# Kernel optimization log

Measured on AMD Instinct MI355X. Metric: run time of the kernel, lower is better.

The kernel has to match this reference:

```python
import jax, jax.numpy as jnp
import numpy as np

NEG = -1e30  # log(0) surrogate, safe for fp32
BLANK = 0
MARGIN = 16.0
EPS = 1e-6  # torch pairwise_distance eps


def ctc_loss(log_probs, labels, input_lengths, label_lengths):
    """Per-sample CTC negative log-likelihood (== nn.CTCLoss(blank=0, reduction='none')).
    log_probs: (T, N, C) log-probabilities; labels: (N, S) int; lengths: (N,).
    """
    T, N, C = log_probs.shape
    S = labels.shape[1]
    L = 2 * S + 1  # extended label length (blanks interleaved)

    # extended labels: blank at even positions, labels at odd positions
    ext = jnp.zeros((N, L), dtype=labels.dtype).at[:, 1::2].set(labels)  # (N, L)
    # skip transition s-2 -> s allowed iff ext[s] != blank and ext[s] != ext[s-2]
    skip = jnp.concatenate(
        [jnp.zeros((N, 2), dtype=bool),
         (ext[:, 2:] != ext[:, :-2]) & (ext[:, 2:] != BLANK)], axis=1)  # (N, L)

    def emit(lp_t):  # lp_t: (N, C) -> (N, L) log-prob of each extended symbol
        return jnp.take_along_axis(lp_t, ext, axis=1)

    # t = 0 init: only positions 0 (blank) and 1 (first label) reachable
    e0 = emit(log_probs[0])
    alpha0 = jnp.full((N, L), NEG).at[:, 0].set(e0[:, 0]).at[:, 1].set(e0[:, 1])

    def step(alpha, xs):
        t, lp_t = xs
        prev1 = jnp.concatenate([jnp.full((N, 1), NEG), alpha[:, :-1]], axis=1)
        prev2 = jnp.concatenate([jnp.full((N, 2), NEG), alpha[:, :-2]], axis=1)
        a = jnp.logaddexp(jnp.logaddexp(alpha, prev1),
                          jnp.where(skip, prev2, NEG)) + emit(lp_t)
        # freeze alpha once t >= input_length (per sample)
        a = jnp.where((t < input_lengths)[:, None], a, alpha)
        return a, None

    ts = jnp.arange(1, T)
    alpha_T, _ = jax.lax.scan(step, alpha0, (ts, log_probs[1:]))

    # final: logaddexp(alpha[2L], alpha[2L-1]) at last valid frame
    idx_hi = (2 * label_lengths)[:, None]
    a_hi = jnp.take_along_axis(alpha_T, idx_hi, axis=1)[:, 0]
    a_lo = jnp.take_along_axis(alpha_T, idx_hi - 1, axis=1)[:, 0]
    return -jnp.logaddexp(a_hi, a_lo)  # (N,)


def setup_inputs() -> dict:
    key = jax.random.key(0)
    k1, k2, k3, k4, k5 = jax.random.split(key, 5)
    T, N, C, S = 1024, 128, 256, 100
    predicts = jax.nn.log_softmax(
        jax.random.normal(k1, (T, N, C), dtype=jnp.float32), axis=-1)
    labels = jax.random.randint(k2, (N, S), 1, C, dtype=jnp.int32)
    ref_labels = jax.random.randint(k3, (N, S), 1, C, dtype=jnp.int32)
    preds_lengths = jnp.full((N,), T, dtype=jnp.int32)
    label_lengths = jax.random.randint(k4, (N,), 50, S + 1, dtype=jnp.int32)
    ref_lengths = jax.random.randint(k5, (N,), 50, S + 1, dtype=jnp.int32)
    return {"predicts": predicts, "labels": labels, "ref_labels": ref_labels,
            "preds_lengths": preds_lengths, "label_lengths": label_lengths,
            "ref_lengths": ref_lengths}


def reference(predicts, labels, ref_labels, preds_lengths, label_lengths, ref_lengths):
    ctc = ctc_loss(predicts, labels, preds_lengths, label_lengths)      # (N,)
    ref = ctc_loss(predicts, ref_labels, preds_lengths, ref_lengths)    # (N,)
    # TripletMarginLoss(margin=16, p=2), anchor = 0, 1-d embeddings:
    # d(a,x) = |0 - x + eps| ; reduction='mean'; .sum() on scalar is identity.
    d_ap = jnp.abs(EPS - ctc)
    d_an = jnp.abs(EPS - ref)
    margin_loss = jnp.mean(jnp.maximum(d_ap - d_an + MARGIN, 0.0))
    return ctc.sum() + margin_loss
```

## Files before the change

kernel.cpp:

```cpp
#include <hip/hip_runtime.h>
#include <math.h>

#define LOG2E 1.4426950408889634f
#define LN2F  0.6931471805599453f
#define NEGB  (-1e30f)

__device__ __forceinline__ float fexp2(float x){ float r; asm("v_exp_f32 %0, %1":"=v"(r):"v"(x)); return r; }
__device__ __forceinline__ float flog2(float x){ float r; asm("v_log_f32 %0, %1":"=v"(r):"v"(x)); return r; }

template<int CTRL>
__device__ __forceinline__ float dppf(float x){
    return __int_as_float(__builtin_amdgcn_update_dpp(0, __float_as_int(x), CTRL, 0xf, 0xf, false));
}

__global__ __launch_bounds__(64) void ctc_scan_kernel(
    const float* __restrict__ lp,
    const int* __restrict__ labels,
    const int* __restrict__ rlabels,
    const int* __restrict__ ilen,
    const int* __restrict__ llen,
    const int* __restrict__ rlen,
    float* __restrict__ loss,
    int T, int N, int C, int S)
{
    const int n    = blockIdx.x >> 1;
    const int sq   = blockIdx.x & 1;
    const int lane = threadIdx.x;

    const int* lab = sq ? rlabels : labels;
    const int  ll  = sq ? rlen[n] : llen[n];
    int Teff = ilen[n]; if (Teff > T) Teff = T;
    const int Tm1 = T - 1;

    int e1 = 0, e3 = 0;
    bool k1 = false, k3 = false;
    {
        int j0 = 2*lane, j1 = 2*lane + 1;
        if (j0 < S){ e1 = lab[n*S + j0]; if (j0 > 0) k1 = (e1 != lab[n*S + j0 - 1]); }
        if (j1 < S){ e3 = lab[n*S + j1]; k3 = (e3 != e1); }
    }
    const float m0 = (2*lane     <= ll) ? 1.f : 0.f;
    const float m2 = (2*lane + 1 <= ll) ? 1.f : 0.f;
    const float b1 = (2*lane     <  ll) ? 0.f : NEGB;
    const float b3 = (2*lane + 1 <  ll) ? 0.f : NEGB;
    const bool bnd = ((lane & 15) == 0) && (lane != 0);

    const size_t NC = (size_t)N * C;
    const float* base = lp + (size_t)n * C;

    float a0, a1, a2 = 0.f, a3 = 0.f;
    {
        float pb0 = fexp2(base[0]  * LOG2E);
        float p10 = fexp2(base[e1] * LOG2E);
        a0 = (lane == 0) ? pb0 : 0.f;
        a1 = (lane == 0) ? p10 : 0.f;
    }
    int E = 0;

    float Rb[4][3], Rx[4][3], Ry[4][3];
#pragma unroll
    for (int q = 0; q < 4; ++q)
#pragma unroll
        for (int u = 0; u < 3; ++u){
            int tt = 1 + q*3 + u; tt = tt < T ? tt : Tm1;
            const float* rp = base + (size_t)tt * NC;
            Rb[q][u] = rp[0] * LOG2E;
            Rx[q][u] = fmaf(rp[e1], LOG2E, b1);
            Ry[q][u] = fmaf(rp[e3], LOG2E, b3);
        }

    auto stepf = [&](float PB, float PX, float PY){
        float pb = fexp2(PB);
        float p1 = fexp2(PX);
        float p3 = fexp2(PY);
        float sh = dppf<0x111>(a3);
        float bc = dppf<0x142>(a3);
        float pa3 = bnd ? bc : sh;
        float v0 = (a0 + pa3) * (pb * m0);
        float v1 = (a1 + a0 + (k1 ? pa3 : 0.f)) * p1;
        float v2 = (a2 + a1) * (pb * m2);
        float v3 = (a3 + a2 + (k3 ? a1 : 0.f)) * p3;
        a0 = v0; a1 = v1; a2 = v2; a3 = v3;
    };

    auto rescale = [&](){
        float m = fmaxf(fmaxf(a0, a1), fmaxf(a2, a3));
        m = fmaxf(m, dppf<0x111>(m));
        m = fmaxf(m, dppf<0x112>(m));
        m = fmaxf(m, dppf<0x114>(m));
        m = fmaxf(m, dppf<0x118>(m));
        m = fmaxf(m, dppf<0x142>(m));
        m = fmaxf(m, dppf<0x143>(m));
        float wmax = __int_as_float(__builtin_amdgcn_readlane(__float_as_int(m), 63));
        int ex = ((__float_as_int(wmax) >> 23) & 255) - 127;
        a0 = ldexpf(a0, -ex); a1 = ldexpf(a1, -ex);
        a2 = ldexpf(a2, -ex); a3 = ldexpf(a3, -ex);
        E += ex;
    };

    int t = 1;
    for (; t + 12 <= Teff; t += 12){
#pragma unroll
        for (int q = 0; q < 4; ++q){
#pragma unroll
            for (int u = 0; u < 3; ++u) stepf(Rb[q][u], Rx[q][u], Ry[q][u]);
#pragma unroll
            for (int u = 0; u < 3; ++u){
                int tt = t + 12 + q*3 + u; tt = tt < T ? tt : Tm1;
                const float* rp = base + (size_t)tt * NC;
                Rb[q][u] = rp[0] * LOG2E;
                Rx[q][u] = fmaf(rp[e1], LOG2E, b1);
                Ry[q][u] = fmaf(rp[e3], LOG2E, b3);
            }
            if (q & 1) rescale();
        }
    }
#pragma unroll
    for (int i = 0; i < 12; ++i){
        if (t + i < Teff) stepf(Rb[i/3][i%3], Rx[i/3][i%3], Ry[i/3][i%3]);
    }

    __shared__ __align__(16) float aout[256];
    reinterpret_cast<float4*>(aout)[lane] = make_float4(a0, a1, a2, a3);
    __syncthreads();
    if (lane == 0){
        float hi = aout[2*ll], lo = aout[2*ll - 1];
        loss[sq * N + n] = -(flog2(hi + lo) + (float)E) * LN2F;
    }
}

__global__ __launch_bounds__(256) void ctc_finalize_kernel(
    const float* __restrict__ ws, float* __restrict__ out, int N)
{
    __shared__ float sc[256], sh[256];
    const int i = threadIdx.x;
    float c = 0.f, h = 0.f;
    for (int nn = i; nn < N; nn += 256) {
        float cv = ws[nn];
        float rv = ws[N + nn];
        c += cv;
        float dap = fabsf(1e-6f - cv);
        float dan = fabsf(1e-6f - rv);
        h += fmaxf(dap - dan + 16.0f, 0.f);
    }
    sc[i] = c; sh[i] = h;
    __syncthreads();
    for (int off = 128; off > 0; off >>= 1) {
        if (i < off) { sc[i] += sc[i + off]; sh[i] += sh[i + off]; }
        __syncthreads();
    }
    if (i == 0) out[0] = sc[0] + sh[0] / (float)N;
}

extern "C" void kernel_launch(void* const* d_in, const int* in_sizes, int n_in,
                              void* d_out, int out_size, void* d_ws, size_t ws_size,
                              hipStream_t stream) {
    const float* lp      = (const float*)d_in[0];
    const int* labels    = (const int*)d_in[1];
    const int* rlabels   = (const int*)d_in[2];
    const int* plen      = (const int*)d_in[3];
    const int* llen      = (const int*)d_in[4];
    const int* rlen      = (const int*)d_in[5];

    const int N = in_sizes[3];
    const int S = in_sizes[1] / N;
    const int C = 256;
    const int T = in_sizes[0] / (N * C);

    float* ws = (float*)d_ws;

    ctc_scan_kernel<<<2 * N, 64, 0, stream>>>(lp, labels, rlabels, plen, llen, rlen,
                                              ws, T, N, C, S);
    ctc_finalize_kernel<<<1, 256, 0, stream>>>(ws, (float*)d_out, N);
}
```

Baseline: 115.6 us.

## Hand-schedule deeper prefetch pipeline with inline asm loads and explicit vmcnt waits

Raises the prefetch depth of log-prob rows from 12 to 18 timesteps and issues the loads through inline-asm global_load_dword with an SGPR base. Partial s_waitcnt vmcnt(45) waits and sched barriers let the recurrence consume the oldest group while later loads stay in flight. The LOG2E scaling and the blank mask fmas move from load time into the step. The aim is to hide global memory latency on the serial scan, at the cost of more registers and fragile hand-tuned wait counts.

```diff
diff --git a/kernel.cpp b/kernel.cpp
--- a/kernel.cpp
+++ b/kernel.cpp
@@ -12,6 +12,16 @@
 __device__ __forceinline__ float dppf(float x){
     return __int_as_float(__builtin_amdgcn_update_dpp(0, __float_as_int(x), CTRL, 0xf, 0xf, false));
 }
+
+__device__ __forceinline__ float gload(const float* sbase, int voff){
+    float r;
+    asm volatile("global_load_dword %0, %1, %2"
+                 : "=v"(r) : "v"(voff), "s"(sbase));
+    return r;
+}
+
+#define WAITV(N) asm volatile("s_waitcnt vmcnt(" #N ")" ::: "memory")
+#define SB0() __builtin_amdgcn_sched_barrier(0)
 
 __global__ __launch_bounds__(64) void ctc_scan_kernel(
     const float* __restrict__ lp,
@@ -47,6 +57,7 @@
 
     const size_t NC = (size_t)N * C;
     const float* base = lp + (size_t)n * C;
+    const int vx = 4*e1, vy = 4*e3, vz = 0;
 
     float a0, a1, a2 = 0.f, a3 = 0.f;
     {
@@ -57,22 +68,25 @@
     }
     int E = 0;
 
-    float Rb[4][3], Rx[4][3], Ry[4][3];
+    asm volatile("s_waitcnt vmcnt(0)" ::: "memory");
+    SB0();
+
+    float Rb[6][3], Rx[6][3], Ry[6][3];
 #pragma unroll
-    for (int q = 0; q < 4; ++q)
+    for (int g = 0; g < 6; ++g)
 #pragma unroll
         for (int u = 0; u < 3; ++u){
-            int tt = 1 + q*3 + u; tt = tt < T ? tt : Tm1;
-            const float* rp = base + (size_t)tt * NC;
-            Rb[q][u] = rp[0] * LOG2E;
-            Rx[q][u] = fmaf(rp[e1], LOG2E, b1);
-            Ry[q][u] = fmaf(rp[e3], LOG2E, b3);
+            int row = 1 + g*3 + u; if (row > Tm1) row = Tm1;
+            const float* rp = base + (size_t)row * NC;
+            Rb[g][u] = gload(rp, vz);
+            Rx[g][u] = gload(rp, vx);
+            Ry[g][u] = gload(rp, vy);
         }
 
     auto stepf = [&](float PB, float PX, float PY){
-        float pb = fexp2(PB);
-        float p1 = fexp2(PX);
-        float p3 = fexp2(PY);
+        float pb = fexp2(PB * LOG2E);
+        float p1 = fexp2(fmaf(PX, LOG2E, b1));
+        float p3 = fexp2(fmaf(PY, LOG2E, b3));
         float sh = dppf<0x111>(a3);
         float bc = dppf<0x142>(a3);
         float pa3 = bnd ? bc : sh;
@@ -99,25 +113,34 @@
     };
 
     int t = 1;
-    for (; t + 12 <= Teff; t += 12){
+    for (; t + 18 <= Teff; t += 18){
 #pragma unroll
-        for (int q = 0; q < 4; ++q){
-#pragma unroll
-            for (int u = 0; u < 3; ++u) stepf(Rb[q][u], Rx[q][u], Ry[q][u]);
+        for (int g = 0; g < 6; ++g){
+            WAITV(45);
+            SB0();
+            stepf(Rb[g][0], Rx[g][0], Ry[g][0]);
+            stepf(Rb[g][1], Rx[g][1], Ry[g][1]);
+            stepf(Rb[g][2], Rx[g][2], Ry[g][2]);
+            if (g & 1) rescale();
 #pragma unroll
             for (int u = 0; u < 3; ++u){
-                int tt = t + 12 + q*3 + u; tt = tt < T ? tt : Tm1;
-                const float* rp = base + (size_t)tt * NC;
-                Rb[q][u] = rp[0] * LOG2E;
-                Rx[q][u] = fmaf(rp[e1], LOG2E, b1);
-                Ry[q][u] = fmaf(rp[e3], LOG2E, b3);
+                int row = t + 18 + g*3 + u; if (row > Tm1) row = Tm1;
+                const float* rp = base + (size_t)row * NC;
+                Rb[g][u] = gload(rp, vz);
+                Rx[g][u] = gload(rp, vx);
+                Ry[g][u] = gload(rp, vy);
             }
-            if (q & 1) rescale();
         }
     }
+
+    WAITV(0);
+    SB0();
 #pragma unroll
-    for (int i = 0; i < 12; ++i){
-        if (t + i < Teff) stepf(Rb[i/3][i%3], Rx[i/3][i%3], Ry[i/3][i%3]);
+    for (int g = 0; g < 6; ++g){
+#pragma unroll
+        for (int u = 0; u < 3; ++u)
+            if (t + g*3 + u < Teff) stepf(Rb[g][u], Rx[g][u], Ry[g][u]);
+        if (t + g*3 < Teff) rescale();
     }
 
     __shared__ __align__(16) float aout[256];
```

Measured after the change: 102.2 us. -11.6%, faster.

## Stage per-timestep log-prob rows into an LDS ring via async global_load_lds

Applied to the files above, without the earlier changes.

Replaces the per-lane register prefetch of scattered gathered log-probs with coalesced async global-to-LDS copies of whole 256-class rows into a 32-deep ring buffer, 24 rows ahead. Each step then reads its blank and label emissions from LDS, with hand-placed waitcnt and sched barriers to overlap loads with the recurrence. The goal is to replace the latency-bound scattered global gathers on the serial critical path. In exchange it relies on fragile manual vmcnt/lgkmcnt counting, loads full rows instead of only the needed entries, and now rescales every 6 steps instead of 2.

```diff
diff --git a/kernel.cpp b/kernel.cpp
--- a/kernel.cpp
+++ b/kernel.cpp
@@ -12,6 +12,16 @@
 __device__ __forceinline__ float dppf(float x){
     return __int_as_float(__builtin_amdgcn_update_dpp(0, __float_as_int(x), CTRL, 0xf, 0xf, false));
 }
+
+__device__ __forceinline__ float ldsread(unsigned addr){
+    float r;
+    asm volatile("ds_read_b32 %0, %1" : "=v"(r) : "v"(addr));
+    return r;
+}
+
+#define WAITV(N) asm volatile("s_waitcnt vmcnt(" #N ")" ::: "memory")
+#define WAITL(N) asm volatile("s_waitcnt lgkmcnt(" #N ")" ::: "memory")
+#define SB0() __builtin_amdgcn_sched_barrier(0)
 
 __global__ __launch_bounds__(64) void ctc_scan_kernel(
     const float* __restrict__ lp,
@@ -32,6 +42,9 @@
     int Teff = ilen[n]; if (Teff > T) Teff = T;
     const int Tm1 = T - 1;
 
+    __shared__ __align__(16) float ring[32][256];
+    __shared__ __align__(16) float aout[256];
+
     int e1 = 0, e3 = 0;
     bool k1 = false, k3 = false;
     {
@@ -47,6 +60,12 @@
 
     const size_t NC = (size_t)N * C;
     const float* base = lp + (size_t)n * C;
+    const float* gsrc = base + lane * 4;
+
+    const unsigned RB = (unsigned)(size_t)(__attribute__((address_space(3))) char*)&ring[0][0];
+    const unsigned ab = RB;
+    const unsigned ax = RB + 4u * (unsigned)e1;
+    const unsigned ay = RB + 4u * (unsigned)e3;
 
     float a0, a1, a2 = 0.f, a3 = 0.f;
     {
@@ -57,22 +76,29 @@
     }
     int E = 0;
 
-    float Rb[4][3], Rx[4][3], Ry[4][3];
-#pragma unroll
-    for (int q = 0; q < 4; ++q)
-#pragma unroll
-        for (int u = 0; u < 3; ++u){
-            int tt = 1 + q*3 + u; tt = tt < T ? tt : Tm1;
-            const float* rp = base + (size_t)tt * NC;
-            Rb[q][u] = rp[0] * LOG2E;
-            Rx[q][u] = fmaf(rp[e1], LOG2E, b1);
-            Ry[q][u] = fmaf(rp[e3], LOG2E, b3);
-        }
-
-    auto stepf = [&](float PB, float PX, float PY){
-        float pb = fexp2(PB);
-        float p1 = fexp2(PX);
-        float p3 = fexp2(PY);
+    asm volatile("s_waitcnt vmcnt(0) lgkmcnt(0)" ::: "memory");
+    SB0();
+
+    auto stage = [&](int row){
+        int rr = row < Tm1 ? row : Tm1;
+        __builtin_amdgcn_global_load_lds(
+            (const __attribute__((address_space(1))) char*)(gsrc + (size_t)rr * NC),
+            (__attribute__((address_space(3))) char*)&ring[row & 31][0],
+            16, 0, 0);
+    };
+
+    float emB[3], emX[3], emY[3];
+    auto issue_reads = [&](int row, int p){
+        unsigned so = (unsigned)((row & 31) << 10);
+        emB[p] = ldsread(ab + so);
+        emX[p] = ldsread(ax + so);
+        emY[p] = ldsread(ay + so);
+    };
+
+    auto stepf = [&](int P){
+        float pb = fexp2(emB[P] * LOG2E);
+        float p1 = fexp2(fmaf(emX[P], LOG2E, b1));
+        float p3 = fexp2(fmaf(emY[P], LOG2E, b3));
         float sh = dppf<0x111>(a3);
         float bc = dppf<0x142>(a3);
         float pa3 = bnd ? bc : sh;
@@ -81,6 +107,15 @@
         float v2 = (a2 + a1) * (pb * m2);
         float v3 = (a3 + a2 + (k3 ? a1 : 0.f)) * p3;
         a0 = v0; a1 = v1; a2 = v2; a3 = v3;
+    };
+
+    auto STEPQ = [&](int tcur, int P, int Pn){
+        stage(tcur + 24);
+        WAITV(22);
+        issue_reads(tcur + 2, Pn);
+        WAITL(6);
+        SB0();
+        stepf(P);
     };
 
     auto rescale = [&](){
@@ -98,29 +133,33 @@
         E += ex;
     };
 
+#pragma unroll
+    for (int r = 1; r <= 24; ++r) stage(r);
+    WAITV(22);
+    issue_reads(1, 1);
+    issue_reads(2, 2);
+
     int t = 1;
-    for (; t + 12 <= Teff; t += 12){
-#pragma unroll
-        for (int q = 0; q < 4; ++q){
-#pragma unroll
-            for (int u = 0; u < 3; ++u) stepf(Rb[q][u], Rx[q][u], Ry[q][u]);
-#pragma unroll
-            for (int u = 0; u < 3; ++u){
-                int tt = t + 12 + q*3 + u; tt = tt < T ? tt : Tm1;
-                const float* rp = base + (size_t)tt * NC;
-                Rb[q][u] = rp[0] * LOG2E;
-                Rx[q][u] = fmaf(rp[e1], LOG2E, b1);
-                Ry[q][u] = fmaf(rp[e3], LOG2E, b3);
-            }
-            if (q & 1) rescale();
-        }
-    }
-#pragma unroll
-    for (int i = 0; i < 12; ++i){
-        if (t + i < Teff) stepf(Rb[i/3][i%3], Rx[i/3][i%3], Ry[i/3][i%3]);
-    }
-
-    __shared__ __align__(16) float aout[256];
+    for (; t + 6 <= Teff; t += 6){
+        STEPQ(t + 0, 1, 0);
+        STEPQ(t + 1, 2, 1);
+        STEPQ(t + 2, 0, 2);
+        STEPQ(t + 3, 1, 0);
+        STEPQ(t + 4, 2, 1);
+        STEPQ(t + 5, 0, 2);
+        rescale();
+    }
+    {
+        if (t + 0 < Teff) STEPQ(t + 0, 1, 0);
+        if (t + 1 < Teff) STEPQ(t + 1, 2, 1);
+        if (t + 2 < Teff) STEPQ(t + 2, 0, 2);
+        if (t + 3 < Teff) STEPQ(t + 3, 1, 0);
+        if (t + 4 < Teff) STEPQ(t + 4, 2, 1);
+    }
+
+    asm volatile("s_waitcnt vmcnt(0) lgkmcnt(0)" ::: "memory");
+    SB0();
+
     reinterpret_cast<float4*>(aout)[lane] = make_float4(a0, a1, a2, a3);
     __syncthreads();
     if (lane == 0){
```

Measured after the change: 124.9 us. +8.0%, slower.

## Use inline-asm global loads with explicit vmcnt waits for software prefetch pipeline

Applied to the files above, without the earlier changes.

Replaces compiler-scheduled prefetch arrays with inline-asm global_load_dword into named registers, explicit s_waitcnt vmcnt(27) before each 3-step group, and sched_barriers. This keeps up to 9 rows of loads in flight and stops the compiler from inserting conservative full waits. The LOG2E scaling and bias moves from load time into the step, so raw loads can land directly in registers. Hand-written waitcnt is fragile, because any extra memory op the compiler emits breaks the counting. The tail now rescales more often.

```diff
diff --git a/kernel.cpp b/kernel.cpp
--- a/kernel.cpp
+++ b/kernel.cpp
@@ -12,6 +12,30 @@
 __device__ __forceinline__ float dppf(float x){
     return __int_as_float(__builtin_amdgcn_update_dpp(0, __float_as_int(x), CTRL, 0xf, 0xf, false));
 }
+
+__device__ __forceinline__ float gload(const float* p){
+    float r;
+    asm volatile("global_load_dword %0, %1, off" : "=v"(r) : "v"(p));
+    return r;
+}
+#define WAITV(N) asm volatile("s_waitcnt vmcnt(" #N ")" ::: "memory")
+#define SB0() __builtin_amdgcn_sched_barrier(0)
+
+#define RESCALE4(x0,x1,x2,x3,E)                                              \
+    {                                                                        \
+        float mx_ = fmaxf(fmaxf(x0,x1), fmaxf(x2,x3));                       \
+        mx_ = fmaxf(mx_, dppf<0x111>(mx_));                                  \
+        mx_ = fmaxf(mx_, dppf<0x112>(mx_));                                  \
+        mx_ = fmaxf(mx_, dppf<0x114>(mx_));                                  \
+        mx_ = fmaxf(mx_, dppf<0x118>(mx_));                                  \
+        mx_ = fmaxf(mx_, dppf<0x142>(mx_));                                  \
+        mx_ = fmaxf(mx_, dppf<0x143>(mx_));                                  \
+        float wm_ = __int_as_float(__builtin_amdgcn_readlane(__float_as_int(mx_), 63)); \
+        int ex_ = ((__float_as_int(wm_) >> 23) & 255) - 127;                 \
+        x0 = ldexpf(x0,-ex_); x1 = ldexpf(x1,-ex_);                          \
+        x2 = ldexpf(x2,-ex_); x3 = ldexpf(x3,-ex_);                          \
+        E += ex_;                                                            \
+    }
 
 __global__ __launch_bounds__(64) void ctc_scan_kernel(
     const float* __restrict__ lp,
@@ -29,20 +53,17 @@
 
     const int* lab = sq ? rlabels : labels;
     const int  ll  = sq ? rlen[n] : llen[n];
-    int Teff = ilen[n]; if (Teff > T) Teff = T;
+    int Teff = ilen[n]; if (Teff > T) Teff = T; if (Teff < 1) Teff = 1;
     const int Tm1 = T - 1;
 
-    int e1 = 0, e3 = 0;
-    bool k1 = false, k3 = false;
-    {
-        int j0 = 2*lane, j1 = 2*lane + 1;
-        if (j0 < S){ e1 = lab[n*S + j0]; if (j0 > 0) k1 = (e1 != lab[n*S + j0 - 1]); }
-        if (j1 < S){ e3 = lab[n*S + j1]; k3 = (e3 != e1); }
-    }
-    const float m0 = (2*lane     <= ll) ? 1.f : 0.f;
-    const float m2 = (2*lane + 1 <= ll) ? 1.f : 0.f;
-    const float b1 = (2*lane     <  ll) ? 0.f : NEGB;
-    const float b3 = (2*lane + 1 <  ll) ? 0.f : NEGB;
+    const int j0 = 2*lane, j1 = 2*lane + 1;
+    int e1 = 0, e3 = 0; bool k1 = false, k3 = false;
+    if (j0 < S){ e1 = lab[n*S + j0]; if (j0 > 0) k1 = (e1 != lab[n*S + j0 - 1]); }
+    if (j1 < S){ e3 = lab[n*S + j1]; k3 = (e3 != e1); }
+    const float m0 = (j0 <= ll) ? 1.f : 0.f;
+    const float m2 = (j1 <= ll) ? 1.f : 0.f;
+    const float b1 = (j0 <  ll) ? 0.f : NEGB;
+    const float b3 = (j1 <  ll) ? 0.f : NEGB;
     const bool bnd = ((lane & 15) == 0) && (lane != 0);
 
     const size_t NC = (size_t)N * C;
@@ -57,22 +78,18 @@
     }
     int E = 0;
 
-    float Rb[4][3], Rx[4][3], Ry[4][3];
-#pragma unroll
-    for (int q = 0; q < 4; ++q)
-#pragma unroll
-        for (int u = 0; u < 3; ++u){
-            int tt = 1 + q*3 + u; tt = tt < T ? tt : Tm1;
-            const float* rp = base + (size_t)tt * NC;
-            Rb[q][u] = rp[0] * LOG2E;
-            Rx[q][u] = fmaf(rp[e1], LOG2E, b1);
-            Ry[q][u] = fmaf(rp[e3], LOG2E, b3);
-        }
+    asm volatile("" :: "v"(m0), "v"(m2), "v"(b1), "v"(b3), "v"(e1), "v"(e3));
+    asm volatile("s_waitcnt vmcnt(0) lgkmcnt(0)" ::: "memory"); SB0();
+
+#define LOAD3(Ba,Xa,Ya,row_) {                                    \
+        int r_ = (row_); if (r_ > Tm1) r_ = Tm1;                  \
+        const float* rp_ = base + (size_t)r_ * NC;                \
+        Ba = gload(rp_); Xa = gload(rp_ + e1); Ya = gload(rp_ + e3); }
 
     auto stepf = [&](float PB, float PX, float PY){
-        float pb = fexp2(PB);
-        float p1 = fexp2(PX);
-        float p3 = fexp2(PY);
+        float pb = fexp2(PB * LOG2E);
+        float p1 = fexp2(fmaf(PX, LOG2E, b1));
+        float p3 = fexp2(fmaf(PY, LOG2E, b3));
         float sh = dppf<0x111>(a3);
         float bc = dppf<0x142>(a3);
         float pa3 = bnd ? bc : sh;
@@ -83,42 +100,55 @@
         a0 = v0; a1 = v1; a2 = v2; a3 = v3;
     };
 
-    auto rescale = [&](){
-        float m = fmaxf(fmaxf(a0, a1), fmaxf(a2, a3));
-        m = fmaxf(m, dppf<0x111>(m));
-        m = fmaxf(m, dppf<0x112>(m));
-        m = fmaxf(m, dppf<0x114>(m));
-        m = fmaxf(m, dppf<0x118>(m));
-        m = fmaxf(m, dppf<0x142>(m));
-        m = fmaxf(m, dppf<0x143>(m));
-        float wmax = __int_as_float(__builtin_amdgcn_readlane(__float_as_int(m), 63));
-        int ex = ((__float_as_int(wmax) >> 23) & 255) - 127;
-        a0 = ldexpf(a0, -ex); a1 = ldexpf(a1, -ex);
-        a2 = ldexpf(a2, -ex); a3 = ldexpf(a3, -ex);
-        E += ex;
-    };
+    float B0a,X0a,Y0a, B0b,X0b,Y0b, B0c,X0c,Y0c;
+    float B1a,X1a,Y1a, B1b,X1b,Y1b, B1c,X1c,Y1c;
+    float B2a,X2a,Y2a, B2b,X2b,Y2b, B2c,X2c,Y2c;
+    float B3a,X3a,Y3a, B3b,X3b,Y3b, B3c,X3c,Y3c;
+
+    LOAD3(B0a,X0a,Y0a, 1);  LOAD3(B0b,X0b,Y0b, 2);  LOAD3(B0c,X0c,Y0c, 3);
+    LOAD3(B1a,X1a,Y1a, 4);  LOAD3(B1b,X1b,Y1b, 5);  LOAD3(B1c,X1c,Y1c, 6);
+    LOAD3(B2a,X2a,Y2a, 7);  LOAD3(B2b,X2b,Y2b, 8);  LOAD3(B2c,X2c,Y2c, 9);
+    LOAD3(B3a,X3a,Y3a,10);  LOAD3(B3b,X3b,Y3b,11);  LOAD3(B3c,X3c,Y3c,12);
 
     int t = 1;
     for (; t + 12 <= Teff; t += 12){
-#pragma unroll
-        for (int q = 0; q < 4; ++q){
-#pragma unroll
-            for (int u = 0; u < 3; ++u) stepf(Rb[q][u], Rx[q][u], Ry[q][u]);
-#pragma unroll
-            for (int u = 0; u < 3; ++u){
-                int tt = t + 12 + q*3 + u; tt = tt < T ? tt : Tm1;
-                const float* rp = base + (size_t)tt * NC;
-                Rb[q][u] = rp[0] * LOG2E;
-                Rx[q][u] = fmaf(rp[e1], LOG2E, b1);
-                Ry[q][u] = fmaf(rp[e3], LOG2E, b3);
-            }
-            if (q & 1) rescale();
-        }
-    }
-#pragma unroll
-    for (int i = 0; i < 12; ++i){
-        if (t + i < Teff) stepf(Rb[i/3][i%3], Rx[i/3][i%3], Ry[i/3][i%3]);
-    }
+        WAITV(27); SB0();
+        stepf(B0a,X0a,Y0a); stepf(B0b,X0b,Y0b); stepf(B0c,X0c,Y0c);
+        LOAD3(B0a,X0a,Y0a, t+12); LOAD3(B0b,X0b,Y0b, t+13); LOAD3(B0c,X0c,Y0c, t+14);
+
+        WAITV(27); SB0();
+        stepf(B1a,X1a,Y1a); stepf(B1b,X1b,Y1b); stepf(B1c,X1c,Y1c);
+        RESCALE4(a0, a1, a2, a3, E);
+        LOAD3(B1a,X1a,Y1a, t+15); LOAD3(B1b,X1b,Y1b, t+16); LOAD3(B1c,X1c,Y1c, t+17);
+
+        WAITV(27); SB0();
+        stepf(B2a,X2a,Y2a); stepf(B2b,X2b,Y2b); stepf(B2c,X2c,Y2c);
+        LOAD3(B2a,X2a,Y2a, t+18); LOAD3(B2b,X2b,Y2b, t+19); LOAD3(B2c,X2c,Y2c, t+20);
+
+        WAITV(27); SB0();
+        stepf(B3a,X3a,Y3a); stepf(B3b,X3b,Y3b); stepf(B3c,X3c,Y3c);
+        RESCALE4(a0, a1, a2, a3, E);
+        LOAD3(B3a,X3a,Y3a, t+21); LOAD3(B3b,X3b,Y3b, t+22); LOAD3(B3c,X3c,Y3c, t+23);
+    }
+
+    WAITV(0); SB0();
+    if (t + 0 < Teff) stepf(B0a,X0a,Y0a);
+    if (t + 1 < Teff) stepf(B0b,X0b,Y0b);
+    if (t + 2 < Teff) stepf(B0c,X0c,Y0c);
+    if (t + 0 < Teff) RESCALE4(a0, a1, a2, a3, E);
+    if (t + 3 < Teff) stepf(B1a,X1a,Y1a);
+    if (t + 4 < Teff) stepf(B1b,X1b,Y1b);
+    if (t + 5 < Teff) stepf(B1c,X1c,Y1c);
+    if (t + 3 < Teff) RESCALE4(a0, a1, a2, a3, E);
+    if (t + 6 < Teff) stepf(B2a,X2a,Y2a);
+    if (t + 7 < Teff) stepf(B2b,X2b,Y2b);
+    if (t + 8 < Teff) stepf(B2c,X2c,Y2c);
+    if (t + 6 < Teff) RESCALE4(a0, a1, a2, a3, E);
+    if (t + 9 < Teff) stepf(B3a,X3a,Y3a);
+    if (t +10 < Teff) stepf(B3b,X3b,Y3b);
+    if (t +11 < Teff) stepf(B3c,X3c,Y3c);
+
+#undef LOAD3
 
     __shared__ __align__(16) float aout[256];
     reinterpret_cast<float4*>(aout)[lane] = make_float4(a0, a1, a2, a3);
```

New measurement: 109.7 us. -5.1%, faster.
